# Kernel optimization log

Measured on AMD Instinct MI355X. Metric: run time of the kernel, lower is better.

## Reference

```python
import jax, jax.numpy as jnp
import numpy as np


def setup_inputs() -> dict:
    key = jax.random.key(0)
    ks = jax.random.split(key, 5)
    b, l, ns, ni, d = 128, 64, 32, 16, 256
    scale = 1.0 / np.sqrt(d)
    return {
        "token_features": jax.random.normal(ks[0], (b, l, d), jnp.float32),
        "w_route_ws": jax.random.normal(ks[1], (l, ns, d), jnp.float32) * scale,
        "w_pose_ws": jax.random.normal(ks[2], (l, ns, d, d), jnp.float32) * scale,
        "w_route_si": jax.random.normal(ks[3], (ns, ni, d), jnp.float32) * scale,
        "w_pose_si": jax.random.normal(ks[4], (ns, ni, d, d), jnp.float32) * scale,
    }


def reference(token_features, w_route_ws, w_pose_ws, w_route_si, w_pose_si):
    d_model = token_features.shape[-1]

    # ---- route words -> slots ----
    # token activations ('norm' strategy): mean over d_model -> (b, l)
    a_words = jnp.sum(token_features, axis=-1) / d_model
    # routing logits (b, l, n_slot_caps), softmax over slot caps
    c_ws = jax.nn.softmax(jnp.einsum('lnj,blj->bln', w_route_ws, token_features), axis=-1)
    weighted_c = jnp.einsum('bls,bl->bs', c_ws, a_words)            # (b, ns)
    a_slots = weighted_c / jnp.sum(a_words, axis=-1, keepdims=True)  # (b, ns)
    # pose votes (b, l, ns, d) then weighted aggregation + divisive normalization
    u_hat_slots = jnp.einsum('lnij,blj->blni', w_pose_ws, token_features)
    u_slots = jnp.einsum('bls,bl,blsk->bsk', c_ws, a_words, u_hat_slots) / weighted_c[:, :, None]

    # ---- route slots -> intents ----
    c_si = jax.nn.softmax(jnp.einsum('sij,bsj->bsi', w_route_si, u_slots), axis=-1)
    weighted_c2 = jnp.einsum('bsi,bs->bi', c_si, a_slots)            # (b, ni)
    a_intents = weighted_c2 / jnp.sum(a_slots, axis=-1, keepdims=True)
    u_hat_intents = jnp.einsum('sijk,bsk->bsik', w_pose_si, u_slots)  # (b, ns, ni, d)
    u_intents = jnp.einsum('bsi,bs,bsik->bik', c_si, a_slots, u_hat_intents) / weighted_c2[:, :, None]

    return a_slots, u_slots, a_intents, u_intents
```

## Files before the change

### kernel.cpp

```cpp
#include <hip/hip_runtime.h>
#include <math.h>

#define B  128
#define L  64
#define NS 32
#define NI 16
#define D  256

typedef __attribute__((ext_vector_type(8))) short bf16x8;
typedef __attribute__((ext_vector_type(4))) float f32x4;

__device__ __forceinline__ float wave_reduce_sum(float v) {
#pragma unroll
  for (int off = 32; off; off >>= 1) v += __shfl_xor(v, off, 64);
  return v;
}
__device__ __forceinline__ float wave_reduce_max(float v) {
#pragma unroll
  for (int off = 32; off; off >>= 1) v = fmaxf(v, __shfl_xor(v, off, 64));
  return v;
}

__device__ __forceinline__ uint cvt_pk_bf16(float a, float b) {
  uint r;
  asm("v_cvt_pk_bf16_f32 %0, %1, %2" : "=v"(r) : "v"(a), "v"(b));
  return r;
}
__device__ __forceinline__ void split4(float4 v, uint2& h, uint2& lo) {
  h.x = cvt_pk_bf16(v.x, v.y);
  h.y = cvt_pk_bf16(v.z, v.w);
  float h0 = __uint_as_float(h.x << 16);
  float h1 = __uint_as_float(h.x & 0xFFFF0000u);
  float h2 = __uint_as_float(h.y << 16);
  float h3 = __uint_as_float(h.y & 0xFFFF0000u);
  lo.x = cvt_pk_bf16(v.x - h0, v.y - h1);
  lo.y = cvt_pk_bf16(v.z - h2, v.w - h3);
}

__device__ __forceinline__ void dma16(const void* g, void* l) {
  __builtin_amdgcn_global_load_lds(
      (const __attribute__((address_space(1))) void*)g,
      (__attribute__((address_space(3))) void*)l, 16, 0, 0);
}

__global__ __launch_bounds__(256) void kx_split(
    const float* __restrict__ tf, ushort* __restrict__ xh,
    ushort* __restrict__ xl) {
  int bx = blockIdx.x;
  int l  = bx >> 2, jp = bx & 3;
  int t  = threadIdx.x;
  int row = t >> 1, sub = t & 1;
  int tile = bx * 2 + sub;
  const float* src = tf + ((size_t)row * L + l) * D + jp * 64 + sub * 32;
  ushort* ht = xh + (size_t)tile * 4096 + row * 32;
  ushort* lt = xl + (size_t)tile * 4096 + row * 32;
#pragma unroll
  for (int u = 0; u < 4; ++u) {
    float4 v0 = *(const float4*)(src + u * 8);
    float4 v1 = *(const float4*)(src + u * 8 + 4);
    uint2 h0, e0, h1, e1;
    split4(v0, h0, e0);
    split4(v1, h1, e1);
    int up = (u ^ (row & 3)) * 8;
    uint4 hu = {h0.x, h0.y, h1.x, h1.y};
    uint4 lu = {e0.x, e0.y, e1.x, e1.y};
    *(uint4*)&ht[up] = hu;
    *(uint4*)&lt[up] = lu;
  }
}

__global__ __launch_bounds__(256) void k1_route_words(
    const float* __restrict__ tf, const float* __restrict__ wr,
    float* __restrict__ wlsT, float* __restrict__ a_words) {
  int bl = blockIdx.x;
  int b  = bl >> 6;
  int l  = bl & (L - 1);
  int t  = threadIdx.x;
  int wave = t >> 6, lane = t & 63;
  __shared__ float sx[D];
  __shared__ float slog[NS];
  __shared__ float s_aw;
  sx[t] = tf[bl * D + t];
  __syncthreads();
  const float* wbase = wr + l * NS * D;
#pragma unroll
  for (int r = 0; r < 8; ++r) {
    int n = wave * 8 + r;
    const float* w = wbase + n * D;
    float p = 0.f;
#pragma unroll
    for (int jj = 0; jj < 4; ++jj) {
      int j = lane + jj * 64;
      p = fmaf(w[j], sx[j], p);
    }
    p = wave_reduce_sum(p);
    if (lane == 0) slog[n] = p;
  }
  if (wave == 0) {
    float p = sx[lane] + sx[lane + 64] + sx[lane + 128] + sx[lane + 192];
    p = wave_reduce_sum(p);
    if (lane == 0) s_aw = p * (1.f / D);
  }
  __syncthreads();
  if (wave == 0) {
    float aw = s_aw;
    float v = (lane < NS) ? slog[lane] : -INFINITY;
    float m = wave_reduce_max(v);
    float e = (lane < NS) ? __expf(v - m) : 0.f;
    float s = wave_reduce_sum(e);
    if (lane < NS) wlsT[(l * NS + lane) * B + b] = (e / s) * aw;
    if (lane == 0) a_words[bl] = aw;
  }
}

__global__ __launch_bounds__(64) void k2_slots_agg(
    const float* __restrict__ wlsT, const float* __restrict__ a_words,
    float* __restrict__ weighted_c, float* __restrict__ a_slots) {
  int b = blockIdx.x;
  int lane = threadIdx.x;
  float aw = a_words[b * L + lane];
  float sa = wave_reduce_sum(aw);
  if (lane < NS) {
    float wc = 0.f;
    for (int l = 0; l < L; ++l) wc += wlsT[(l * NS + lane) * B + b];
    weighted_c[b * NS + lane] = wc;
    a_slots[b * NS + lane] = wc / sa;
  }
}

__global__ __launch_bounds__(256, 2) void k3_mfma(
    const ushort* __restrict__ xh, const ushort* __restrict__ xl,
    const float* __restrict__ wp, const float* __restrict__ wlsT,
    float* __restrict__ part, int nsplit) {
  __shared__ ushort Ah[2][4096], Al[2][4096];
  __shared__ float  Wt[2][4096];
  __shared__ float  swl[2][256];

  int bx  = blockIdx.x;
  int sp  = bx & (nsplit - 1);
  int rem = bx / nsplit;
  int ih  = rem & 1, s = rem >> 1;
  int i0  = ih * 128;
  int lchunk = L / nsplit, l0 = sp * lchunk;
  int steps  = lchunk * 8;

  int t = threadIdx.x, lane = t & 63, wv = t >> 6;
  int fr = lane & 15, q = lane >> 4;
  int wrow8 = lane >> 3;
  int wu    = lane & 7;
  int wswz  = ((wu ^ wrow8) << 4);

  f32x4 P[8][2], R[8][2];
#pragma unroll
  for (int mi = 0; mi < 8; ++mi)
#pragma unroll
    for (int ni = 0; ni < 2; ++ni) { P[mi][ni] = (f32x4)0.f; R[mi][ni] = (f32x4)0.f; }

  auto issue = [&](int tn) {
    int cs = tn < steps ? tn : steps - 1;
    int pb = tn & 1;
    int li = cs >> 3, jci = cs & 7;
    int l  = l0 + li;
    const ushort* th = xh + ((size_t)l * 8 + jci) * 4096;
    const ushort* tl = xl + ((size_t)l * 8 + jci) * 4096;
    dma16(th + wv * 1024 + lane * 8,       &Ah[pb][wv * 1024]);
    dma16(th + wv * 1024 + 512 + lane * 8, &Ah[pb][wv * 1024 + 512]);
    dma16(tl + wv * 1024 + lane * 8,       &Al[pb][wv * 1024]);
    dma16(tl + wv * 1024 + 512 + lane * 8, &Al[pb][wv * 1024 + 512]);
    const char* wb = (const char*)wp +
                     (((size_t)l * NS + s) * (D * D) + (size_t)i0 * D) * 4 +
                     jci * 128;
#pragma unroll
    for (int wi = 0; wi < 4; ++wi) {
      int rbase = wv * 32 + wi * 8;
      dma16(wb + (size_t)(rbase + wrow8) * 1024 + wswz,
            (char*)&Wt[pb][0] + rbase * 128);
    }
    const char* sws = (const char*)(wlsT + ((size_t)l * NS + s) * B);
    dma16(sws + lane * 16, &swl[(cs >> 3) & 1][0]);
  };

  issue(0);
  for (int tt = 0; tt < steps; ++tt) {
    issue(tt + 1);
    asm volatile("s_waitcnt vmcnt(9)" ::: "memory");
    __builtin_amdgcn_s_barrier();
    int pb = tt & 1;
    bf16x8 fh[2], fl[2];
#pragma unroll
    for (int ni = 0; ni < 2; ++ni) {
      int wr = wv * 32 + ni * 16 + fr;
      const char* wbp = (const char*)&Wt[pb][0] + wr * 128;
      int key = fr & 7;
      float4 w0 = *(const float4*)(wbp + (((q * 2 + 0) ^ key) << 4));
      float4 w1 = *(const float4*)(wbp + (((q * 2 + 1) ^ key) << 4));
      uint2 h0, e0, h1, e1;
      split4(w0, h0, e0);
      split4(w1, h1, e1);
      uint4 hu = {h0.x, h0.y, h1.x, h1.y};
      uint4 lu = {e0.x, e0.y, e1.x, e1.y};
      fh[ni] = __builtin_bit_cast(bf16x8, hu);
      fl[ni] = __builtin_bit_cast(bf16x8, lu);
    }
#pragma unroll
    for (int mi = 0; mi < 8; ++mi) {
      int ar = mi * 16 + fr;
      int au = ar * 32 + ((q ^ (fr & 3)) << 3);
      bf16x8 ah = *(const bf16x8*)&Ah[pb][au];
      bf16x8 al = *(const bf16x8*)&Al[pb][au];
#pragma unroll
      for (int ni = 0; ni < 2; ++ni) {
        P[mi][ni] = __builtin_amdgcn_mfma_f32_16x16x32_bf16(ah, fh[ni], P[mi][ni], 0, 0, 0);
        P[mi][ni] = __builtin_amdgcn_mfma_f32_16x16x32_bf16(ah, fl[ni], P[mi][ni], 0, 0, 0);
        P[mi][ni] = __builtin_amdgcn_mfma_f32_16x16x32_bf16(al, fh[ni], P[mi][ni], 0, 0, 0);
      }
    }
    if ((tt & 7) == 7) {
      int lb = (tt >> 3) & 1;
#pragma unroll
      for (int mi = 0; mi < 8; ++mi) {
        f32x4 s4 = *(const f32x4*)&swl[lb][mi * 16 + q * 4];
#pragma unroll
        for (int ni = 0; ni < 2; ++ni) {
          R[mi][ni] += s4 * P[mi][ni];
          P[mi][ni] = (f32x4)0.f;
        }
      }
    }
    asm volatile("s_waitcnt lgkmcnt(0)" ::: "memory");
    __builtin_amdgcn_s_barrier();
  }

  float* pout = part + ((size_t)sp * NS + s) * (B * D);
#pragma unroll
  for (int mi = 0; mi < 8; ++mi)
#pragma unroll
    for (int ni = 0; ni < 2; ++ni) {
      int col = i0 + wv * 32 + ni * 16 + fr;
#pragma unroll
      for (int e = 0; e < 4; ++e) {
        int bb = mi * 16 + q * 4 + e;
        pout[(size_t)bb * D + col] = R[mi][ni][e];
      }
    }
}

__global__ __launch_bounds__(256) void k3r_reduce(
    const float* __restrict__ part, const float* __restrict__ wc,
    float* __restrict__ u_slots, int nsplit) {
  int idx = blockIdx.x * 256 + threadIdx.x;
  int i  = idx & (D - 1);
  int sb = idx >> 8;
  int b  = sb & (B - 1);
  int s  = sb >> 7;
  float v = 0.f;
  for (int sp = 0; sp < nsplit; ++sp)
    v += part[(size_t)sp * (NS * B * D) + idx];
  u_slots[((size_t)b * NS + s) * D + i] = v / wc[b * NS + s];
}

__global__ __launch_bounds__(64) void k4_route_si(
    const float* __restrict__ u_slots, const float* __restrict__ wr_si,
    const float* __restrict__ a_slots, float* __restrict__ w2) {
  int bs = blockIdx.x;
  int s  = bs & (NS - 1);
  int lane = threadIdx.x;
  __shared__ float su[D];
  __shared__ float slog[NI];
#pragma unroll
  for (int jj = 0; jj < 4; ++jj) su[lane + jj * 64] = u_slots[bs * D + lane + jj * 64];
  __syncthreads();
  for (int i = 0; i < NI; ++i) {
    const float* w = wr_si + (s * NI + i) * D;
    float p = 0.f;
#pragma unroll
    for (int jj = 0; jj < 4; ++jj) {
      int j = lane + jj * 64;
      p = fmaf(w[j], su[j], p);
    }
    p = wave_reduce_sum(p);
    if (lane == 0) slog[i] = p;
  }
  __syncthreads();
  float v = (lane < NI) ? slog[lane] : -INFINITY;
  float m = wave_reduce_max(v);
  float e = (lane < NI) ? __expf(v - m) : 0.f;
  float ssum = wave_reduce_sum(e);
  if (lane < NI) w2[bs * NI + lane] = (e / ssum) * a_slots[bs];
}

__global__ __launch_bounds__(64) void k5_intents_agg(
    const float* __restrict__ w2, const float* __restrict__ a_slots,
    float* __restrict__ wc2, float* __restrict__ a_intents) {
  int b = blockIdx.x;
  int lane = threadIdx.x;
  float as = (lane < NS) ? a_slots[b * NS + lane] : 0.f;
  float sas = wave_reduce_sum(as);
  if (lane < NI) {
    float wc = 0.f;
    for (int s = 0; s < NS; ++s) wc += w2[(b * NS + s) * NI + lane];
    wc2[b * NI + lane] = wc;
    a_intents[b * NI + lane] = wc / sas;
  }
}

__global__ __launch_bounds__(256) void k6_wsum(
    const float* __restrict__ wps, float* __restrict__ wsum) {
  __shared__ float red[4][D];
  int si = blockIdx.x;
  int t  = threadIdx.x;
  int k4 = (t & 63) * 4;
  int jg = t >> 6;
  const float* base = wps + (size_t)si * D * D;
  float4 acc = {0.f, 0.f, 0.f, 0.f};
  for (int j = jg; j < D; j += 4) {
    float4 v = *(const float4*)(base + (size_t)j * D + k4);
    acc.x += v.x; acc.y += v.y; acc.z += v.z; acc.w += v.w;
  }
  *(float4*)&red[jg][k4] = acc;
  __syncthreads();
  wsum[si * D + t] = (red[0][t] + red[1][t]) + (red[2][t] + red[3][t]);
}

__global__ __launch_bounds__(256) void k7_uintents(
    const float* __restrict__ u_slots, const float* __restrict__ w2,
    const float* __restrict__ wsum, const float* __restrict__ wc2,
    float* __restrict__ u_intents) {
  int bi = blockIdx.x;
  int b = bi >> 4, i = bi & (NI - 1);
  int k = threadIdx.x;
  float acc = 0.f;
  for (int s = 0; s < NS; ++s) {
    float w = w2[(b * NS + s) * NI + i];
    acc = fmaf(w * u_slots[(b * NS + s) * D + k], wsum[(s * NI + i) * D + k], acc);
  }
  u_intents[bi * D + k] = acc / wc2[bi];
}

extern "C" void kernel_launch(void* const* d_in, const int* in_sizes, int n_in,
                              void* d_out, int out_size, void* d_ws, size_t ws_size,
                              hipStream_t stream) {
  const float* tf    = (const float*)d_in[0];
  const float* wr_ws = (const float*)d_in[1];
  const float* wp_ws = (const float*)d_in[2];
  const float* wr_si = (const float*)d_in[3];
  const float* wp_si = (const float*)d_in[4];

  float* out       = (float*)d_out;
  float* a_slots   = out;
  float* u_slots   = a_slots + B * NS;
  float* a_intents = u_slots + B * NS * D;
  float* u_intents = a_intents + B * NI;

  float* ws         = (float*)d_ws;
  float* wlsT       = ws;
  float* a_words    = wlsT + L * NS * B;
  float* weighted_c = a_words + B * L;
  float* w2         = weighted_c + B * NS;
  float* wc2        = w2 + B * NS * NI;
  float* wsum       = wc2 + B * NI;
  ushort* xh        = (ushort*)(wsum + NS * NI * D);
  ushort* xl        = xh + (size_t)L * 8 * 4096;
  float*  part      = (float*)(xl + (size_t)L * 8 * 4096);

  const size_t base_f  = 473088 + 2097152;
  const size_t chunk_f = (size_t)NS * B * D;
  size_t avail_f = ws_size / sizeof(float);
  int nsplit = 1;
  if (avail_f >= base_f + 8 * chunk_f)      nsplit = 8;
  else if (avail_f >= base_f + 4 * chunk_f) nsplit = 4;
  else if (avail_f >= base_f + 2 * chunk_f) nsplit = 2;

  kx_split<<<L * 4, 256, 0, stream>>>(tf, xh, xl);
  k1_route_words<<<B * L, 256, 0, stream>>>(tf, wr_ws, wlsT, a_words);
  k2_slots_agg<<<B, 64, 0, stream>>>(wlsT, a_words, weighted_c, a_slots);
  k3_mfma<<<NS * 2 * nsplit, 256, 0, stream>>>(xh, xl, wp_ws, wlsT, part, nsplit);
  k3r_reduce<<<(NS * B * D) / 256, 256, 0, stream>>>(part, weighted_c, u_slots, nsplit);
  k6_wsum<<<NS * NI, 256, 0, stream>>>(wp_si, wsum);
  k4_route_si<<<B * NS, 64, 0, stream>>>(u_slots, wr_si, a_slots, w2);
  k5_intents_agg<<<B, 64, 0, stream>>>(w2, a_slots, wc2, a_intents);
  k7_uintents<<<B * NI, 256, 0, stream>>>(u_slots, w2, wsum, wc2, u_intents);
}
```

Baseline: 244.4 us.

## Restructure k3 MFMA tiling so each wave owns batch rows and reuses X tiles

Reorganises the main pose-vote GEMM kernel so each wave computes 32 batch rows across all 128 output columns instead of 32 columns across all 128 batch rows. The X (token) tiles widen to 64-wide K chunks, load once per four W steps and stay resident, while W loads in smaller 32-row pieces through a 4-deep buffer with two steps of lookahead. The input split kernel changes to the new 64-wide swizzled tile layout. The aim is fewer redundant X reloads and deeper prefetch of the dominant W stream. The cost is more complex barrier and wait-count bookkeeping and the risk of stalls when X tiles reload between groups.

```diff
diff --git a/kernel.cpp b/kernel.cpp
--- a/kernel.cpp
+++ b/kernel.cpp
@@ -46,14 +46,13 @@
 __global__ __launch_bounds__(256) void kx_split(
     const float* __restrict__ tf, ushort* __restrict__ xh,
     ushort* __restrict__ xl) {
-  int bx = blockIdx.x;
-  int l  = bx >> 2, jp = bx & 3;
-  int t  = threadIdx.x;
-  int row = t >> 1, sub = t & 1;
-  int tile = bx * 2 + sub;
-  const float* src = tf + ((size_t)row * L + l) * D + jp * 64 + sub * 32;
-  ushort* ht = xh + (size_t)tile * 4096 + row * 32;
-  ushort* lt = xl + (size_t)tile * 4096 + row * 32;
+  int tile = blockIdx.x;
+  int l = tile >> 2, kq = tile & 3;
+  int t = threadIdx.x;
+  int row = t >> 1, half = t & 1;
+  const float* src = tf + ((size_t)row * L + l) * D + kq * 64 + half * 32;
+  ushort* ht = xh + (size_t)tile * 8192 + row * 64;
+  ushort* lt = xl + (size_t)tile * 8192 + row * 64;
 #pragma unroll
   for (int u = 0; u < 4; ++u) {
     float4 v0 = *(const float4*)(src + u * 8);
@@ -61,11 +60,11 @@
     uint2 h0, e0, h1, e1;
     split4(v0, h0, e0);
     split4(v1, h1, e1);
-    int up = (u ^ (row & 3)) * 8;
+    int gu = (half * 4 + u) ^ (row & 7);
     uint4 hu = {h0.x, h0.y, h1.x, h1.y};
     uint4 lu = {e0.x, e0.y, e1.x, e1.y};
-    *(uint4*)&ht[up] = hu;
-    *(uint4*)&lt[up] = lu;
+    *(uint4*)&ht[gu * 8] = hu;
+    *(uint4*)&lt[gu * 8] = lu;
   }
 }
 
@@ -132,9 +131,9 @@
     const ushort* __restrict__ xh, const ushort* __restrict__ xl,
     const float* __restrict__ wp, const float* __restrict__ wlsT,
     float* __restrict__ part, int nsplit) {
-  __shared__ ushort Ah[2][4096], Al[2][4096];
-  __shared__ float  Wt[2][4096];
-  __shared__ float  swl[2][256];
+  __shared__ ushort Ah[8192], Al[8192];
+  __shared__ float  Wt[4][2048];
+  __shared__ float  swb[2][256];
 
   int bx  = blockIdx.x;
   int sp  = bx & (nsplit - 1);
@@ -142,105 +141,131 @@
   int ih  = rem & 1, s = rem >> 1;
   int i0  = ih * 128;
   int lchunk = L / nsplit, l0 = sp * lchunk;
-  int steps  = lchunk * 8;
+  int steps  = lchunk * 16;
 
   int t = threadIdx.x, lane = t & 63, wv = t >> 6;
   int fr = lane & 15, q = lane >> 4;
-  int wrow8 = lane >> 3;
-  int wu    = lane & 7;
-  int wswz  = ((wu ^ wrow8) << 4);
-
-  f32x4 P[8][2], R[8][2];
-#pragma unroll
-  for (int mi = 0; mi < 8; ++mi)
-#pragma unroll
-    for (int ni = 0; ni < 2; ++ni) { P[mi][ni] = (f32x4)0.f; R[mi][ni] = (f32x4)0.f; }
-
-  auto issue = [&](int tn) {
-    int cs = tn < steps ? tn : steps - 1;
-    int pb = tn & 1;
-    int li = cs >> 3, jci = cs & 7;
+
+  f32x4 P[2][8], R[2][8];
+#pragma unroll
+  for (int mi = 0; mi < 2; ++mi)
+#pragma unroll
+    for (int n = 0; n < 8; ++n) { P[mi][n] = (f32x4)0.f; R[mi][n] = (f32x4)0.f; }
+
+  auto issueW = [&](int n) {
+    int pb = n & 3;
+    int cs = n < steps ? n : steps - 1;
+    int li = cs >> 4, kq = (cs >> 2) & 3, ic = cs & 3;
     int l  = l0 + li;
-    const ushort* th = xh + ((size_t)l * 8 + jci) * 4096;
-    const ushort* tl = xl + ((size_t)l * 8 + jci) * 4096;
-    dma16(th + wv * 1024 + lane * 8,       &Ah[pb][wv * 1024]);
-    dma16(th + wv * 1024 + 512 + lane * 8, &Ah[pb][wv * 1024 + 512]);
-    dma16(tl + wv * 1024 + lane * 8,       &Al[pb][wv * 1024]);
-    dma16(tl + wv * 1024 + 512 + lane * 8, &Al[pb][wv * 1024 + 512]);
-    const char* wb = (const char*)wp +
-                     (((size_t)l * NS + s) * (D * D) + (size_t)i0 * D) * 4 +
-                     jci * 128;
-#pragma unroll
-    for (int wi = 0; wi < 4; ++wi) {
-      int rbase = wv * 32 + wi * 8;
-      dma16(wb + (size_t)(rbase + wrow8) * 1024 + wswz,
-            (char*)&Wt[pb][0] + rbase * 128);
-    }
-    const char* sws = (const char*)(wlsT + ((size_t)l * NS + s) * B);
-    dma16(sws + lane * 16, &swl[(cs >> 3) & 1][0]);
+    const char* base = (const char*)wp +
+        (((size_t)l * NS + s) * (D * D) + (size_t)(i0 + ic * 32) * D + kq * 64) * 4;
+    int r4 = lane >> 4, v = lane & 15;
+#pragma unroll
+    for (int wi = 0; wi < 2; ++wi) {
+      int rb = wv * 8 + wi * 4;
+      const char* src = base + (size_t)(rb + r4) * 1024 +
+                        ((v ^ ((rb + r4) & 7)) << 4);
+      dma16(src, (char*)&Wt[pb][0] + rb * 256);
+    }
   };
-
-  issue(0);
-  for (int tt = 0; tt < steps; ++tt) {
-    issue(tt + 1);
-    asm volatile("s_waitcnt vmcnt(9)" ::: "memory");
-    __builtin_amdgcn_s_barrier();
-    int pb = tt & 1;
-    bf16x8 fh[2], fl[2];
-#pragma unroll
-    for (int ni = 0; ni < 2; ++ni) {
-      int wr = wv * 32 + ni * 16 + fr;
-      const char* wbp = (const char*)&Wt[pb][0] + wr * 128;
-      int key = fr & 7;
-      float4 w0 = *(const float4*)(wbp + (((q * 2 + 0) ^ key) << 4));
-      float4 w1 = *(const float4*)(wbp + (((q * 2 + 1) ^ key) << 4));
-      uint2 h0, e0, h1, e1;
-      split4(w0, h0, e0);
-      split4(w1, h1, e1);
-      uint4 hu = {h0.x, h0.y, h1.x, h1.y};
-      uint4 lu = {e0.x, e0.y, e1.x, e1.y};
-      fh[ni] = __builtin_bit_cast(bf16x8, hu);
-      fl[ni] = __builtin_bit_cast(bf16x8, lu);
-    }
-#pragma unroll
-    for (int mi = 0; mi < 8; ++mi) {
-      int ar = mi * 16 + fr;
-      int au = ar * 32 + ((q ^ (fr & 3)) << 3);
-      bf16x8 ah = *(const bf16x8*)&Ah[pb][au];
-      bf16x8 al = *(const bf16x8*)&Al[pb][au];
+  auto issueA = [&](int li, int kq) {
+    size_t tile = ((size_t)(l0 + li) * 4 + kq) * 8192;
+#pragma unroll
+    for (int c = 0; c < 4; ++c) {
+      dma16(xh + tile + wv * 2048 + c * 512 + lane * 8, &Ah[wv * 2048 + c * 512]);
+      dma16(xl + tile + wv * 2048 + c * 512 + lane * 8, &Al[wv * 2048 + c * 512]);
+    }
+  };
+  auto issueSW = [&](int li) {
+    const char* src = (const char*)(wlsT + ((size_t)(l0 + li) * NS + s) * B);
+    dma16(src + lane * 16, &swb[li & 1][0]);
+  };
+
+  issueA(0, 0);
+  issueSW(0);
+  issueW(0);
+  issueW(1);
+
+  int ngroups = steps >> 2;
+  for (int g = 0; g < ngroups; ++g) {
+#pragma unroll
+    for (int ic = 0; ic < 4; ++ic) {
+      int st = g * 4 + ic;
+      issueW(st + 2);
+      asm volatile("s_waitcnt vmcnt(4)" ::: "memory");
+      __builtin_amdgcn_s_barrier();
+      int pb = st & 3;
+      bf16x8 wh[2][2], wl[2][2];
 #pragma unroll
       for (int ni = 0; ni < 2; ++ni) {
-        P[mi][ni] = __builtin_amdgcn_mfma_f32_16x16x32_bf16(ah, fh[ni], P[mi][ni], 0, 0, 0);
-        P[mi][ni] = __builtin_amdgcn_mfma_f32_16x16x32_bf16(ah, fl[ni], P[mi][ni], 0, 0, 0);
-        P[mi][ni] = __builtin_amdgcn_mfma_f32_16x16x32_bf16(al, fh[ni], P[mi][ni], 0, 0, 0);
-      }
-    }
-    if ((tt & 7) == 7) {
-      int lb = (tt >> 3) & 1;
-#pragma unroll
-      for (int mi = 0; mi < 8; ++mi) {
-        f32x4 s4 = *(const f32x4*)&swl[lb][mi * 16 + q * 4];
-#pragma unroll
-        for (int ni = 0; ni < 2; ++ni) {
-          R[mi][ni] += s4 * P[mi][ni];
-          P[mi][ni] = (f32x4)0.f;
+        int r = ni * 16 + fr;
+        const char* rbp = (const char*)&Wt[pb][0] + r * 256;
+        int key = r & 7;
+#pragma unroll
+        for (int k2 = 0; k2 < 2; ++k2) {
+          float4 w0 = *(const float4*)(rbp + (((k2 * 8 + q * 2 + 0) ^ key) << 4));
+          float4 w1 = *(const float4*)(rbp + (((k2 * 8 + q * 2 + 1) ^ key) << 4));
+          uint2 h0, e0, h1, e1;
+          split4(w0, h0, e0);
+          split4(w1, h1, e1);
+          uint4 hu = {h0.x, h0.y, h1.x, h1.y};
+          uint4 lu = {e0.x, e0.y, e1.x, e1.y};
+          wh[ni][k2] = __builtin_bit_cast(bf16x8, hu);
+          wl[ni][k2] = __builtin_bit_cast(bf16x8, lu);
         }
       }
-    }
-    asm volatile("s_waitcnt lgkmcnt(0)" ::: "memory");
-    __builtin_amdgcn_s_barrier();
+#pragma unroll
+      for (int k2 = 0; k2 < 2; ++k2) {
+#pragma unroll
+        for (int mi = 0; mi < 2; ++mi) {
+          int ar = wv * 32 + mi * 16 + fr;
+          int au = ar * 64 + (((k2 * 4 + q) ^ (ar & 7)) << 3);
+          bf16x8 ah = *(const bf16x8*)&Ah[au];
+          bf16x8 al = *(const bf16x8*)&Al[au];
+#pragma unroll
+          for (int ni = 0; ni < 2; ++ni) {
+            P[mi][ic * 2 + ni] = __builtin_amdgcn_mfma_f32_16x16x32_bf16(
+                ah, wh[ni][k2], P[mi][ic * 2 + ni], 0, 0, 0);
+            P[mi][ic * 2 + ni] = __builtin_amdgcn_mfma_f32_16x16x32_bf16(
+                ah, wl[ni][k2], P[mi][ic * 2 + ni], 0, 0, 0);
+            P[mi][ic * 2 + ni] = __builtin_amdgcn_mfma_f32_16x16x32_bf16(
+                al, wh[ni][k2], P[mi][ic * 2 + ni], 0, 0, 0);
+          }
+        }
+      }
+      asm volatile("s_waitcnt lgkmcnt(0)" ::: "memory");
+      __builtin_amdgcn_s_barrier();
+    }
+    int li = g >> 2, kq = g & 3;
+    if (kq == 3) {
+#pragma unroll
+      for (int mi = 0; mi < 2; ++mi) {
+        f32x4 s4 = *(const f32x4*)&swb[li & 1][wv * 32 + mi * 16 + q * 4];
+#pragma unroll
+        for (int n = 0; n < 8; ++n) {
+          R[mi][n] += s4 * P[mi][n];
+          P[mi][n] = (f32x4)0.f;
+        }
+      }
+      if (li + 1 < lchunk) {
+        issueA(li + 1, 0);
+        issueSW(li + 1);
+      }
+    } else {
+      issueA(li, kq + 1);
+    }
   }
 
   float* pout = part + ((size_t)sp * NS + s) * (B * D);
 #pragma unroll
-  for (int mi = 0; mi < 8; ++mi)
-#pragma unroll
-    for (int ni = 0; ni < 2; ++ni) {
-      int col = i0 + wv * 32 + ni * 16 + fr;
+  for (int mi = 0; mi < 2; ++mi)
+#pragma unroll
+    for (int n = 0; n < 8; ++n) {
+      int col = i0 + n * 16 + fr;
 #pragma unroll
       for (int e = 0; e < 4; ++e) {
-        int bb = mi * 16 + q * 4 + e;
-        pout[(size_t)bb * D + col] = R[mi][ni][e];
+        int bb = wv * 32 + mi * 16 + q * 4 + e;
+        pout[(size_t)bb * D + col] = R[mi][n][e];
       }
     }
 }
@@ -360,8 +385,8 @@
   float* wc2        = w2 + B * NS * NI;
   float* wsum       = wc2 + B * NI;
   ushort* xh        = (ushort*)(wsum + NS * NI * D);
-  ushort* xl        = xh + (size_t)L * 8 * 4096;
-  float*  part      = (float*)(xl + (size_t)L * 8 * 4096);
+  ushort* xl        = xh + (size_t)L * 4 * 8192;
+  float*  part      = (float*)(xl + (size_t)L * 4 * 8192);
 
   const size_t base_f  = 473088 + 2097152;
   const size_t chunk_f = (size_t)NS * B * D;
```

Result: slower. 286.0 us (+17.0%).

## Switch pose GEMM to 32x32x16 MFMA with 2x2 wave tiling

Applied to the files above, without the earlier changes.

Replaces the 16x16x32 bf16 MFMA tiling (each wave covering all 128 batch rows by 32 output columns) with 32x32x16 MFMA instructions on a 2x2 wave grid, each wave owning a 64x64 output tile. This cuts LDS fragment reads per MFMA and uses the larger MFMA shape to reduce instruction issue overhead. The LDS swizzle key for the activation tiles changes to match the new read pattern, and the epilogue and per-token scaling are adapted to the 32x32 accumulator layout. The split-bf16 three-product precision scheme is unchanged.

```diff
diff --git a/kernel.cpp b/kernel.cpp
--- a/kernel.cpp
+++ b/kernel.cpp
@@ -9,6 +9,7 @@
 
 typedef __attribute__((ext_vector_type(8))) short bf16x8;
 typedef __attribute__((ext_vector_type(4))) float f32x4;
+typedef __attribute__((ext_vector_type(16))) float f32x16;
 
 __device__ __forceinline__ float wave_reduce_sum(float v) {
 #pragma unroll
@@ -51,9 +52,10 @@
   int t  = threadIdx.x;
   int row = t >> 1, sub = t & 1;
   int tile = bx * 2 + sub;
-  const float* src = tf + ((size_t)row * L + l) * D + jp * 64 + sub * 32;
+  const float* src = tf + ((size_t)row * L + l) * D + (jp * 2 + sub) * 32;
   ushort* ht = xh + (size_t)tile * 4096 + row * 32;
   ushort* lt = xl + (size_t)tile * 4096 + row * 32;
+  int key = (row >> 1) & 3;
 #pragma unroll
   for (int u = 0; u < 4; ++u) {
     float4 v0 = *(const float4*)(src + u * 8);
@@ -61,7 +63,7 @@
     uint2 h0, e0, h1, e1;
     split4(v0, h0, e0);
     split4(v1, h1, e1);
-    int up = (u ^ (row & 3)) * 8;
+    int up = (u ^ key) * 8;
     uint4 hu = {h0.x, h0.y, h1.x, h1.y};
     uint4 lu = {e0.x, e0.y, e1.x, e1.y};
     *(uint4*)&ht[up] = hu;
@@ -145,20 +147,18 @@
   int steps  = lchunk * 8;
 
   int t = threadIdx.x, lane = t & 63, wv = t >> 6;
-  int fr = lane & 15, q = lane >> 4;
-  int wrow8 = lane >> 3;
-  int wu    = lane & 7;
-  int wswz  = ((wu ^ wrow8) << 4);
-
-  f32x4 P[8][2], R[8][2];
-#pragma unroll
-  for (int mi = 0; mi < 8; ++mi)
-#pragma unroll
-    for (int ni = 0; ni < 2; ++ni) { P[mi][ni] = (f32x4)0.f; R[mi][ni] = (f32x4)0.f; }
+  int wm = wv >> 1, wn = wv & 1;
+  int c31 = lane & 31, q2 = lane >> 5;
+
+  f32x16 P[2][2], R[2][2];
+#pragma unroll
+  for (int mt = 0; mt < 2; ++mt)
+#pragma unroll
+    for (int nt = 0; nt < 2; ++nt) { P[mt][nt] = (f32x16)0.f; R[mt][nt] = (f32x16)0.f; }
 
   auto issue = [&](int tn) {
+    int pb = tn & 1;
     int cs = tn < steps ? tn : steps - 1;
-    int pb = tn & 1;
     int li = cs >> 3, jci = cs & 7;
     int l  = l0 + li;
     const ushort* th = xh + ((size_t)l * 8 + jci) * 4096;
@@ -170,6 +170,8 @@
     const char* wb = (const char*)wp +
                      (((size_t)l * NS + s) * (D * D) + (size_t)i0 * D) * 4 +
                      jci * 128;
+    int wrow8 = lane >> 3, wu = lane & 7;
+    int wswz  = ((wu ^ wrow8) << 4);
 #pragma unroll
     for (int wi = 0; wi < 4; ++wi) {
       int rbase = wv * 32 + wi * 8;
@@ -186,44 +188,58 @@
     asm volatile("s_waitcnt vmcnt(9)" ::: "memory");
     __builtin_amdgcn_s_barrier();
     int pb = tt & 1;
-    bf16x8 fh[2], fl[2];
-#pragma unroll
-    for (int ni = 0; ni < 2; ++ni) {
-      int wr = wv * 32 + ni * 16 + fr;
-      const char* wbp = (const char*)&Wt[pb][0] + wr * 128;
-      int key = fr & 7;
-      float4 w0 = *(const float4*)(wbp + (((q * 2 + 0) ^ key) << 4));
-      float4 w1 = *(const float4*)(wbp + (((q * 2 + 1) ^ key) << 4));
-      uint2 h0, e0, h1, e1;
-      split4(w0, h0, e0);
-      split4(w1, h1, e1);
-      uint4 hu = {h0.x, h0.y, h1.x, h1.y};
-      uint4 lu = {e0.x, e0.y, e1.x, e1.y};
-      fh[ni] = __builtin_bit_cast(bf16x8, hu);
-      fl[ni] = __builtin_bit_cast(bf16x8, lu);
-    }
-#pragma unroll
-    for (int mi = 0; mi < 8; ++mi) {
-      int ar = mi * 16 + fr;
-      int au = ar * 32 + ((q ^ (fr & 3)) << 3);
-      bf16x8 ah = *(const bf16x8*)&Ah[pb][au];
-      bf16x8 al = *(const bf16x8*)&Al[pb][au];
-#pragma unroll
-      for (int ni = 0; ni < 2; ++ni) {
-        P[mi][ni] = __builtin_amdgcn_mfma_f32_16x16x32_bf16(ah, fh[ni], P[mi][ni], 0, 0, 0);
-        P[mi][ni] = __builtin_amdgcn_mfma_f32_16x16x32_bf16(ah, fl[ni], P[mi][ni], 0, 0, 0);
-        P[mi][ni] = __builtin_amdgcn_mfma_f32_16x16x32_bf16(al, fh[ni], P[mi][ni], 0, 0, 0);
+    bf16x8 wh[2][2], wlo[2][2];
+#pragma unroll
+    for (int nt = 0; nt < 2; ++nt) {
+      int wr = wn * 64 + nt * 32 + c31;
+      const char* rb = (const char*)&Wt[pb][0] + wr * 128;
+      int key = wr & 7;
+#pragma unroll
+      for (int kh = 0; kh < 2; ++kh) {
+        int u0 = kh * 4 + q2 * 2;
+        float4 w0 = *(const float4*)(rb + (((u0    ) ^ key) << 4));
+        float4 w1 = *(const float4*)(rb + (((u0 + 1) ^ key) << 4));
+        uint2 h0, e0, h1, e1;
+        split4(w0, h0, e0);
+        split4(w1, h1, e1);
+        uint4 hu = {h0.x, h0.y, h1.x, h1.y};
+        uint4 lu = {e0.x, e0.y, e1.x, e1.y};
+        wh[nt][kh]  = __builtin_bit_cast(bf16x8, hu);
+        wlo[nt][kh] = __builtin_bit_cast(bf16x8, lu);
+      }
+    }
+#pragma unroll
+    for (int mt = 0; mt < 2; ++mt) {
+      int ar   = wm * 64 + mt * 32 + c31;
+      int akey = (ar >> 1) & 3;
+#pragma unroll
+      for (int kh = 0; kh < 2; ++kh) {
+        int au = ar * 32 + (((kh * 2 + q2) ^ akey) << 3);
+        bf16x8 a_h = *(const bf16x8*)&Ah[pb][au];
+        bf16x8 a_l = *(const bf16x8*)&Al[pb][au];
+#pragma unroll
+        for (int nt = 0; nt < 2; ++nt) {
+          P[mt][nt] = __builtin_amdgcn_mfma_f32_32x32x16_bf16(a_h, wh[nt][kh],  P[mt][nt], 0, 0, 0);
+          P[mt][nt] = __builtin_amdgcn_mfma_f32_32x32x16_bf16(a_h, wlo[nt][kh], P[mt][nt], 0, 0, 0);
+          P[mt][nt] = __builtin_amdgcn_mfma_f32_32x32x16_bf16(a_l, wh[nt][kh],  P[mt][nt], 0, 0, 0);
+        }
       }
     }
     if ((tt & 7) == 7) {
       int lb = (tt >> 3) & 1;
 #pragma unroll
-      for (int mi = 0; mi < 8; ++mi) {
-        f32x4 s4 = *(const f32x4*)&swl[lb][mi * 16 + q * 4];
-#pragma unroll
-        for (int ni = 0; ni < 2; ++ni) {
-          R[mi][ni] += s4 * P[mi][ni];
-          P[mi][ni] = (f32x4)0.f;
+      for (int mt = 0; mt < 2; ++mt) {
+        int rbase = wm * 64 + mt * 32 + 4 * q2;
+#pragma unroll
+        for (int g = 0; g < 4; ++g) {
+          f32x4 s4 = *(const f32x4*)&swl[lb][rbase + g * 8];
+#pragma unroll
+          for (int nt = 0; nt < 2; ++nt)
+#pragma unroll
+            for (int w = 0; w < 4; ++w) {
+              R[mt][nt][g * 4 + w] += s4[w] * P[mt][nt][g * 4 + w];
+              P[mt][nt][g * 4 + w] = 0.f;
+            }
         }
       }
     }
@@ -233,14 +249,14 @@
 
   float* pout = part + ((size_t)sp * NS + s) * (B * D);
 #pragma unroll
-  for (int mi = 0; mi < 8; ++mi)
-#pragma unroll
-    for (int ni = 0; ni < 2; ++ni) {
-      int col = i0 + wv * 32 + ni * 16 + fr;
-#pragma unroll
-      for (int e = 0; e < 4; ++e) {
-        int bb = mi * 16 + q * 4 + e;
-        pout[(size_t)bb * D + col] = R[mi][ni][e];
+  for (int mt = 0; mt < 2; ++mt)
+#pragma unroll
+    for (int nt = 0; nt < 2; ++nt) {
+      int col = i0 + wn * 64 + nt * 32 + c31;
+#pragma unroll
+      for (int r = 0; r < 16; ++r) {
+        int row = wm * 64 + mt * 32 + (r & 3) + 8 * (r >> 2) + 4 * q2;
+        pout[(size_t)row * D + col] = R[mt][nt][r];
       }
     }
 }
```

Measured after the change: 251.1 us. 1.03x slower.
